# Optimization experiments

Measured on AMD Instinct MI355X. Metric: run time of the kernel, lower is better.

The kernel has to match this reference:

```python
import jax, jax.numpy as jnp
import numpy as np

N, F_IN, H, C, E = 100000, 512, 16, 40, 3200000
EPS = 1e-5


def setup_inputs() -> dict:
    key = jax.random.key(0)
    ks = jax.random.split(key, 8)
    x = jax.random.normal(ks[0], (N, F_IN), dtype=jnp.float32)
    edge_index = jax.random.randint(ks[1], (2, E), 0, N, dtype=jnp.int64)
    s1 = 1.0 / np.sqrt(F_IN)
    s2 = 1.0 / np.sqrt(H)
    W1 = jax.random.uniform(ks[2], (F_IN, H), jnp.float32, -s1, s1)
    b1 = jnp.zeros((H,), jnp.float32)
    W2 = jax.random.uniform(ks[3], (H, C), jnp.float32, -s2, s2)
    b2 = jnp.zeros((C,), jnp.float32)
    gamma = jnp.ones((H,), jnp.float32)
    beta = jnp.zeros((H,), jnp.float32)
    return {"x": x, "edge_index": edge_index, "W1": W1, "b1": b1,
            "W2": W2, "b2": b2, "gamma": gamma, "beta": beta}


def gcn_conv(x, edge_index, W, b):
    # PyG GCNConv: linear transform, add self-loops, symmetric normalization,
    # scatter-add aggregation at target nodes (edge_index[1]).
    xw = x @ W  # [N, out]
    loops = jnp.arange(N, dtype=edge_index.dtype)
    row = jnp.concatenate([edge_index[0], loops])  # sources
    col = jnp.concatenate([edge_index[1], loops])  # targets
    deg = jax.ops.segment_sum(jnp.ones_like(col, dtype=xw.dtype), col, num_segments=N)
    dis = jnp.where(deg > 0, jax.lax.rsqrt(deg), 0.0)
    norm = dis[row] * dis[col]  # [E+N]
    msgs = norm[:, None] * xw[row]
    out = jax.ops.segment_sum(msgs, col, num_segments=N)
    return out + b


def batch_norm(x, gamma, beta):
    mean = jnp.mean(x, axis=0)
    var = jnp.var(x, axis=0)
    return (x - mean) * jax.lax.rsqrt(var + EPS) * gamma + beta


def reference(x, edge_index, W1, b1, W2, b2, gamma, beta):
    h = jax.nn.relu(gcn_conv(x, edge_index, W1, b1))
    h = batch_norm(h, gamma, beta)
    # dropout omitted (deterministic reference / eval)
    h = gcn_conv(h, edge_index, W2, b2)
    return jax.nn.log_softmax(h, axis=1)
```

## Files before the change

### kernel.cpp

```cpp
#include <hip/hip_runtime.h>

#define NN 100000
#define FIN 512
#define HD 16
#define CD 40
#define NE 3200000
#define EPSV 1e-5f
#define NBUK 391
#define CAP 9216
#define CH 4096
#define NBLK_CNT ((NE + CH - 1) / CH)
#define NBLK_MM ((NN / 16 + 3) / 4)
#define NSTAT 256
#define SMEM_BYTES 37504

typedef __attribute__((ext_vector_type(8))) short short8;
typedef __attribute__((ext_vector_type(4))) float f32x4;

static __device__ __forceinline__ short f2bf(float f) {
  union { float f; unsigned u; } a; a.f = f;
  unsigned r = a.u + 0x7fffu + ((a.u >> 16) & 1u);
  return (short)(r >> 16);
}
static __device__ __forceinline__ float bf2f(unsigned short u) {
  union { unsigned u; float f; } a; a.u = (unsigned)u << 16; return a.f;
}
static __device__ __forceinline__ float2 bfp2f(unsigned p) {
  union { unsigned u; float f; } lo, hi;
  lo.u = p << 16;
  hi.u = p & 0xFFFF0000u;
  return make_float2(lo.f, hi.f);
}
static __device__ __forceinline__ void gload_lds(const float* g, float* l) {
  __builtin_amdgcn_global_load_lds(
      (const __attribute__((address_space(1))) void*)g,
      (__attribute__((address_space(3))) void*)l, 16, 0, 0);
}

__global__ void k_init(int* __restrict__ bkcur, int* __restrict__ gbase) {
  int i = threadIdx.x;
  if (i < NBUK) bkcur[i] = 0;
  if (i == 0) *gbase = 0;
}

__global__ void __launch_bounds__(256) k_fat(const int* __restrict__ ei,
                                             int* __restrict__ bkcur,
                                             unsigned* __restrict__ part,
                                             const float* __restrict__ x,
                                             const float* __restrict__ W1,
                                             float* __restrict__ xw) {
  __shared__ __align__(16) char smem_u[SMEM_BYTES];
  int t = threadIdx.x;
  if (blockIdx.x % 3 == 0) {
    unsigned* stg   = (unsigned*)smem_u;
    unsigned* spk   = stg + CH;
    int*      hist  = (int*)(spk + CH);
    int*      lbase = hist + NBUK;
    int*      gb    = lbase + NBUK + 1;
    int pb = blockIdx.x / 3;
    int e0 = pb * CH;
    int n = NE - e0; if (n > CH) n = CH;
    for (int i = t; i < NBUK; i += 256) hist[i] = 0;
    for (int i = t; i < n; i += 256) stg[i] = (unsigned)ei[NE + e0 + i];
    __syncthreads();
    for (int i = t; i < n; i += 256) atomicAdd(&hist[stg[i] >> 8], 1);
    __syncthreads();
    if (t < 64) {
      int c0 = t * 7;
      int loc[7]; int s = 0;
#pragma unroll
      for (int k = 0; k < 7; k++) {
        int idx = c0 + k;
        int v = (idx < NBUK) ? hist[idx] : 0;
        loc[k] = s; s += v;
      }
      int inc = s;
#pragma unroll
      for (int m = 1; m < 64; m <<= 1) {
        int u = __shfl_up(inc, m);
        if (t >= m) inc += u;
      }
      int base0 = inc - s;
#pragma unroll
      for (int k = 0; k < 7; k++) {
        int idx = c0 + k;
        if (idx < NBUK) lbase[idx] = base0 + loc[k];
      }
      if (t == 63) lbase[NBUK] = base0 + s;
    }
    __syncthreads();
    for (int i = t; i < NBUK; i += 256) {
      int c = hist[i];
      gb[i] = (c > 0) ? atomicAdd(&bkcur[i], c) : 0;
    }
    __syncthreads();
    for (int i = t; i < NBUK; i += 256) hist[i] = lbase[i];
    __syncthreads();
    for (int i = t; i < n; i += 256) {
      unsigned tg = stg[i];
      int b = tg >> 8;
      int pos = atomicAdd(&hist[b], 1);
      spk[pos] = (unsigned)ei[e0 + i] | ((tg & 255u) << 20);
    }
    __syncthreads();
    for (int b = t; b < NBUK; b += 256) {
      int s0 = lbase[b], s1 = lbase[b + 1];
      for (int j = s0; j < s1; j++) stg[j] = (unsigned)b;
    }
    __syncthreads();
    for (int i = t; i < n; i += 256) {
      int b = (int)stg[i];
      int slot = gb[b] + (i - lbase[b]);
      if (slot < CAP) part[(size_t)b * CAP + slot] = spk[i];
    }
  } else {
    int mb = blockIdx.x - blockIdx.x / 3 - 1;
    int wave = t >> 6;
    int lane = t & 63;
    int tile = mb * 4 + wave;
    int row0 = tile * 16;
    if (row0 >= NN) return;
    int lr = lane & 15;
    int kg = lane >> 4;
    float* xs = (float*)smem_u + wave * 2048;

    short8 bfrag[16];
#pragma unroll
    for (int s = 0; s < 16; s++) {
      int kbase = s * 32 + kg * 8;
      short8 bf;
#pragma unroll
      for (int i = 0; i < 8; i++) bf[i] = f2bf(W1[(kbase + i) * HD + lr]);
      bfrag[s] = bf;
    }

    const float* xbase = x + (size_t)row0 * FIN;
    int rr = lane >> 4;
    int pos = lane & 15;
#define STAGE(c)                                                         \
    {                                                                    \
      float* dst = xs + ((c) & 1) * 1024;                                \
      _Pragma("unroll")                                                  \
      for (int j = 0; j < 4; j++) {                                      \
        int row = j * 4 + rr;                                            \
        int u = (pos - row) & 15;                                        \
        gload_lds(xbase + (size_t)row * FIN + (c) * 64 + u * 4,          \
                  dst + j * 256);                                        \
      }                                                                  \
    }

    STAGE(0);
    STAGE(1);
    f32x4 acc = {0.f, 0.f, 0.f, 0.f};
#pragma unroll
    for (int c = 0; c < 8; c++) {
      if (c < 7) { asm volatile("s_waitcnt vmcnt(4)" ::: "memory"); }
      else       { asm volatile("s_waitcnt vmcnt(0)" ::: "memory"); }
      __builtin_amdgcn_sched_barrier(0);
      const float* bufp = xs + (c & 1) * 1024;
#pragma unroll
      for (int s2 = 0; s2 < 2; s2++) {
        int lu0 = s2 * 8 + 2 * kg;
        f32x4 u0 = *(const f32x4*)(bufp + lr * 64 + ((lu0 + lr) & 15) * 4);
        f32x4 u1 = *(const f32x4*)(bufp + lr * 64 + ((lu0 + 1 + lr) & 15) * 4);
        short8 af;
        af[0] = f2bf(u0.x); af[1] = f2bf(u0.y); af[2] = f2bf(u0.z); af[3] = f2bf(u0.w);
        af[4] = f2bf(u1.x); af[5] = f2bf(u1.y); af[6] = f2bf(u1.z); af[7] = f2bf(u1.w);
        acc = __builtin_amdgcn_mfma_f32_16x16x32_bf16(af, bfrag[c * 2 + s2], acc, 0, 0, 0);
      }
      __builtin_amdgcn_sched_barrier(0);
      if (c < 6) STAGE(c + 2);
    }
#undef STAGE
#pragma unroll
    for (int i = 0; i < 4; i++)
      xw[(size_t)(row0 + kg * 4 + i) * HD + lr] = acc[i];
  }
}

__global__ void __launch_bounds__(1024) k_bucket(const int* __restrict__ bkcur,
                                                 const unsigned* __restrict__ part,
                                                 const float* __restrict__ xw,
                                                 int* __restrict__ gbase,
                                                 int* __restrict__ off,
                                                 int* __restrict__ offe,
                                                 float* __restrict__ dis,
                                                 unsigned short* __restrict__ y1b,
                                                 int* __restrict__ srcs) {
  __shared__ unsigned ssrc[CAP];
  __shared__ int lh[256];
  __shared__ int lb[256];
  __shared__ int base_s;
  int b = blockIdx.x, t = threadIdx.x;
  int cnt = bkcur[b]; if (cnt > CAP) cnt = CAP;
  const unsigned* bp = part + (size_t)b * CAP;
  if (t < 256) lh[t] = 0;
  __syncthreads();
  for (int i = t; i < cnt; i += 1024) atomicAdd(&lh[(bp[i] >> 20) & 255], 1);
  __syncthreads();
  int h = 0;
  if (t < 256) { h = lh[t]; lb[t] = h; }
  __syncthreads();
  for (int d = 1; d < 256; d <<= 1) {
    int u = (t < 256 && t >= d) ? lb[t - d] : 0;
    __syncthreads();
    if (t < 256) lb[t] += u;
    __syncthreads();
  }
  if (t == 255) base_s = atomicAdd(gbase, lb[255]);
  __syncthreads();
  int base = base_s;
  if (t < 256) {
    int excl = lb[t] - h;
    int node = (b << 8) + t;
    if (node < NN) {
      off[node] = base + excl;
      offe[node] = base + excl + h;
      float d = rsqrtf((float)(1 + h));
      dis[node] = d;
      const f32x4* xp = (const f32x4*)(xw + (size_t)node * HD);
      f32x4 v0 = xp[0] * d, v1 = xp[1] * d, v2 = xp[2] * d, v3 = xp[3] * d;
      short8 r0, r1;
      r0[0] = f2bf(v0.x); r0[1] = f2bf(v0.y); r0[2] = f2bf(v0.z); r0[3] = f2bf(v0.w);
      r0[4] = f2bf(v1.x); r0[5] = f2bf(v1.y); r0[6] = f2bf(v1.z); r0[7] = f2bf(v1.w);
      r1[0] = f2bf(v2.x); r1[1] = f2bf(v2.y); r1[2] = f2bf(v2.z); r1[3] = f2bf(v2.w);
      r1[4] = f2bf(v3.x); r1[5] = f2bf(v3.y); r1[6] = f2bf(v3.z); r1[7] = f2bf(v3.w);
      short8* yp = (short8*)(y1b + (size_t)node * HD);
      yp[0] = r0; yp[1] = r1;
    }
    lh[t] = excl;
  }
  __syncthreads();
  for (int i = t; i < cnt; i += 1024) {
    unsigned p = bp[i];
    int pos = atomicAdd(&lh[(p >> 20) & 255], 1);
    ssrc[pos] = p & 0xFFFFFu;
  }
  __syncthreads();
  for (int i = t; i < cnt; i += 1024) srcs[base + i] = (int)ssrc[i];
}

__global__ void __launch_bounds__(256) k_g1(const int* __restrict__ off,
                                            const int* __restrict__ offe,
                                            const int* __restrict__ srcs,
                                            const float* __restrict__ dis,
                                            const unsigned short* __restrict__ y1b,
                                            const float* __restrict__ b1,
                                            float* __restrict__ h) {
  int node = (blockIdx.x * blockDim.x + threadIdx.x) >> 6;
  if (node >= NN) return;
  int lane = threadIdx.x & 63;
  int cp = lane & 7;
  int g = lane >> 3;
  int start = off[node], end = offe[node];
  const unsigned* y1u = (const unsigned*)y1b;
  float ax = 0.f, ay = 0.f;
  int i = start + g;
  for (; i + 24 < end; i += 32) {
    int r0 = srcs[i];
    int r1 = srcs[i + 8];
    int r2 = srcs[i + 16];
    int r3 = srcs[i + 24];
    float2 p0 = bfp2f(y1u[(size_t)r0 * 8 + cp]);
    float2 p1 = bfp2f(y1u[(size_t)r1 * 8 + cp]);
    float2 p2 = bfp2f(y1u[(size_t)r2 * 8 + cp]);
    float2 p3 = bfp2f(y1u[(size_t)r3 * 8 + cp]);
    ax += (p0.x + p1.x) + (p2.x + p3.x);
    ay += (p0.y + p1.y) + (p2.y + p3.y);
  }
  for (; i < end; i += 8) {
    float2 p = bfp2f(y1u[(size_t)srcs[i] * 8 + cp]);
    ax += p.x; ay += p.y;
  }
#pragma unroll
  for (int m = 8; m < 64; m <<= 1) {
    ax += __shfl_xor(ax, m);
    ay += __shfl_xor(ay, m);
  }
  if (g == 0) {
    float d = dis[node];
    float2 pn = bfp2f(y1u[(size_t)node * 8 + cp]);
    float vx = d * (pn.x + ax) + b1[2 * cp];
    float vy = d * (pn.y + ay) + b1[2 * cp + 1];
    float2* hp = (float2*)(h + (size_t)node * HD);
    hp[cp] = make_float2(fmaxf(vx, 0.f), fmaxf(vy, 0.f));
  }
}

__global__ void __launch_bounds__(256) k_stats(const float* __restrict__ h,
                                               float* __restrict__ partial) {
  __shared__ float wsum[4][32];
  int stride = gridDim.x * blockDim.x;
  int t0 = blockIdx.x * blockDim.x + threadIdx.x;
  f32x4 s = {0.f, 0.f, 0.f, 0.f}, s2 = {0.f, 0.f, 0.f, 0.f};
  for (int t = t0; t < NN * 4; t += stride) {
    f32x4 v = ((const f32x4*)h)[t];
    s += v; s2 += v * v;
  }
#pragma unroll
  for (int m = 4; m < 64; m <<= 1) {
    s.x += __shfl_xor(s.x, m);  s.y += __shfl_xor(s.y, m);
    s.z += __shfl_xor(s.z, m);  s.w += __shfl_xor(s.w, m);
    s2.x += __shfl_xor(s2.x, m); s2.y += __shfl_xor(s2.y, m);
    s2.z += __shfl_xor(s2.z, m); s2.w += __shfl_xor(s2.w, m);
  }
  int wave = threadIdx.x >> 6, lane = threadIdx.x & 63;
  if (lane < 4) {
    int cb = lane * 4;
    wsum[wave][cb + 0] = s.x;  wsum[wave][cb + 1] = s.y;
    wsum[wave][cb + 2] = s.z;  wsum[wave][cb + 3] = s.w;
    wsum[wave][16 + cb + 0] = s2.x; wsum[wave][16 + cb + 1] = s2.y;
    wsum[wave][16 + cb + 2] = s2.z; wsum[wave][16 + cb + 3] = s2.w;
  }
  __syncthreads();
  if (threadIdx.x < 32) {
    float a = ((wsum[0][threadIdx.x] + wsum[1][threadIdx.x]) +
               (wsum[2][threadIdx.x] + wsum[3][threadIdx.x]));
    partial[blockIdx.x * 32 + threadIdx.x] = a;
  }
}

__global__ void __launch_bounds__(256) k_y2(const float* __restrict__ h,
                                            const float* __restrict__ partial,
                                            const float* __restrict__ gamma,
                                            const float* __restrict__ beta,
                                            const float* __restrict__ dis,
                                            unsigned short* __restrict__ y2b) {
  __shared__ float raw[32];
  __shared__ float scs[16], shs[16];
  int j = threadIdx.x;
  if (j < 32) {
    float a = 0.f;
    for (int b = 0; b < NSTAT; b++) a += partial[b * 32 + j];
    raw[j] = a;
  }
  __syncthreads();
  if (j < 16) {
    float mean = raw[j] * (1.0f / NN);
    float var = raw[16 + j] * (1.0f / NN) - mean * mean;
    float inv = rsqrtf(var + EPSV);
    float sc = gamma[j] * inv;
    scs[j] = sc;
    shs[j] = beta[j] - mean * sc;
  }
  __syncthreads();
  int node = blockIdx.x * blockDim.x + j;
  if (node >= NN) return;
  float d = dis[node];
  const f32x4* hp = (const f32x4*)(h + (size_t)node * HD);
  const f32x4* scp = (const f32x4*)scs;
  const f32x4* shp = (const f32x4*)shs;
  f32x4 v0 = (hp[0] * scp[0] + shp[0]) * d;
  f32x4 v1 = (hp[1] * scp[1] + shp[1]) * d;
  f32x4 v2 = (hp[2] * scp[2] + shp[2]) * d;
  f32x4 v3 = (hp[3] * scp[3] + shp[3]) * d;
  short8 r0, r1;
  r0[0] = f2bf(v0.x); r0[1] = f2bf(v0.y); r0[2] = f2bf(v0.z); r0[3] = f2bf(v0.w);
  r0[4] = f2bf(v1.x); r0[5] = f2bf(v1.y); r0[6] = f2bf(v1.z); r0[7] = f2bf(v1.w);
  r1[0] = f2bf(v2.x); r1[1] = f2bf(v2.y); r1[2] = f2bf(v2.z); r1[3] = f2bf(v2.w);
  r1[4] = f2bf(v3.x); r1[5] = f2bf(v3.y); r1[6] = f2bf(v3.z); r1[7] = f2bf(v3.w);
  short8* yp = (short8*)(y2b + (size_t)node * HD);
  yp[0] = r0; yp[1] = r1;
}

__global__ void __launch_bounds__(256) k_g2(const int* __restrict__ off,
                                            const int* __restrict__ offe,
                                            const int* __restrict__ srcs,
                                            const float* __restrict__ dis,
                                            const unsigned short* __restrict__ y2b,
                                            const float* __restrict__ W2,
                                            const float* __restrict__ b2,
                                            float* __restrict__ out) {
  int node = (blockIdx.x * blockDim.x + threadIdx.x) >> 6;
  if (node >= NN) return;
  int lane = threadIdx.x & 63;
  int cp = lane & 7;
  int g = lane >> 3;
  int start = off[node], end = offe[node];
  const unsigned* y2u = (const unsigned*)y2b;
  float ax = 0.f, ay = 0.f;
  int i = start + g;
  for (; i + 24 < end; i += 32) {
    int r0 = srcs[i];
    int r1 = srcs[i + 8];
    int r2 = srcs[i + 16];
    int r3 = srcs[i + 24];
    float2 p0 = bfp2f(y2u[(size_t)r0 * 8 + cp]);
    float2 p1 = bfp2f(y2u[(size_t)r1 * 8 + cp]);
    float2 p2 = bfp2f(y2u[(size_t)r2 * 8 + cp]);
    float2 p3 = bfp2f(y2u[(size_t)r3 * 8 + cp]);
    ax += (p0.x + p1.x) + (p2.x + p3.x);
    ay += (p0.y + p1.y) + (p2.y + p3.y);
  }
  for (; i < end; i += 8) {
    float2 p = bfp2f(y2u[(size_t)srcs[i] * 8 + cp]);
    ax += p.x; ay += p.y;
  }
#pragma unroll
  for (int m = 8; m < 64; m <<= 1) {
    ax += __shfl_xor(ax, m);
    ay += __shfl_xor(ay, m);
  }
  float d = dis[node];
  float2 pn = bfp2f(y2u[(size_t)node * 8 + cp]);
  float rx = d * (pn.x + ax);
  float ry = d * (pn.y + ay);
  int cls = lane;
  float z = (cls < CD) ? b2[cls] : 0.f;
#pragma unroll
  for (int k = 0; k < 8; k++) {
    float rkx = __shfl(rx, k);
    float rky = __shfl(ry, k);
    if (cls < CD) {
      z += rkx * W2[(2 * k) * CD + cls];
      z += rky * W2[(2 * k + 1) * CD + cls];
    }
  }
  float zz = (cls < CD) ? z : -1e30f;
#pragma unroll
  for (int m = 1; m < 64; m <<= 1) zz = fmaxf(zz, __shfl_xor(zz, m));
  float e = (cls < CD) ? __expf(z - zz) : 0.f;
#pragma unroll
  for (int m = 1; m < 64; m <<= 1) e += __shfl_xor(e, m);
  float l = __logf(e) + zz;
  if (cls < CD) out[(size_t)node * CD + cls] = z - l;
}

extern "C" void kernel_launch(void* const* d_in, const int* in_sizes, int n_in,
                              void* d_out, int out_size, void* d_ws, size_t ws_size,
                              hipStream_t stream) {
  const float* x     = (const float*)d_in[0];
  const int*   ei    = (const int*)d_in[1];
  const float* W1    = (const float*)d_in[2];
  const float* b1    = (const float*)d_in[3];
  const float* W2    = (const float*)d_in[4];
  const float* b2    = (const float*)d_in[5];
  const float* gamma = (const float*)d_in[6];
  const float* beta  = (const float*)d_in[7];
  float* out = (float*)d_out;

  float* ws = (float*)d_ws;
  float*          dis     = ws;
  float*          partial = ws + NN;
  float*          xw      = partial + NSTAT * 32;
  unsigned short* y1b     = (unsigned short*)(xw + (size_t)NN * HD);
  float*          h       = (float*)(y1b + (size_t)NN * HD);
  unsigned short* y2b     = (unsigned short*)(h + (size_t)NN * HD);
  int*            off     = (int*)(y2b + (size_t)NN * HD);
  int*            offe    = off + NN;
  int*            srcs    = offe + NN;
  int*            bkcur   = srcs + NE;
  int*            gbase   = bkcur + NBUK;
  unsigned*       part    = (unsigned*)(gbase + 1);

  const int nblk_n   = (NN + 255) / 256;
  const int nblk_gw  = (NN * 64 + 255) / 256;
  const int nblk_fat = NBLK_CNT + NBLK_MM;

  k_init<<<1, 512, 0, stream>>>(bkcur, gbase);
  k_fat<<<nblk_fat, 256, 0, stream>>>(ei, bkcur, part, x, W1, xw);
  k_bucket<<<NBUK, 1024, 0, stream>>>(bkcur, part, xw, gbase, off, offe, dis, y1b, srcs);
  k_g1<<<nblk_gw, 256, 0, stream>>>(off, offe, srcs, dis, y1b, b1, h);
  k_stats<<<NSTAT, 256, 0, stream>>>(h, partial);
  k_y2<<<nblk_n, 256, 0, stream>>>(h, partial, gamma, beta, dis, y2b);
  k_g2<<<nblk_gw, 256, 0, stream>>>(off, offe, srcs, dis, y2b, W2, b2, out);
}
```

Measured before the change: 215.6 us.

## Shrink fused kernel shared memory: direct atomic scatter and smaller x staging chunks

The edge-partition blocks drop the local prefix-scan and staging pass. They now reserve global bucket offsets per block and scatter each edge directly using a shared atomic slot counter, so spk, lbase and gb are no longer needed. The matmul blocks stage 32-column chunks of x, down from 64, in a smaller double buffer and run 16 pipeline steps with a tighter vmcnt. Both changes cut shared memory per block roughly in half to allow more resident blocks. The cost is less locally coalesced global writes to part, since writes are no longer grouped by bucket, and shallower prefetch per stage.

```diff
diff --git a/kernel.cpp b/kernel.cpp
--- a/kernel.cpp
+++ b/kernel.cpp
@@ -12,7 +12,7 @@
 #define NBLK_CNT ((NE + CH - 1) / CH)
 #define NBLK_MM ((NN / 16 + 3) / 4)
 #define NSTAT 256
-#define SMEM_BYTES 37504
+#define SMEM_BYTES 17952
 
 typedef __attribute__((ext_vector_type(8))) short short8;
 typedef __attribute__((ext_vector_type(4))) float f32x4;
@@ -52,11 +52,8 @@
   __shared__ __align__(16) char smem_u[SMEM_BYTES];
   int t = threadIdx.x;
   if (blockIdx.x % 3 == 0) {
-    unsigned* stg   = (unsigned*)smem_u;
-    unsigned* spk   = stg + CH;
-    int*      hist  = (int*)(spk + CH);
-    int*      lbase = hist + NBUK;
-    int*      gb    = lbase + NBUK + 1;
+    unsigned* stg  = (unsigned*)smem_u;
+    int*      hist = (int*)(stg + CH);
     int pb = blockIdx.x / 3;
     int e0 = pb * CH;
     int n = NE - e0; if (n > CH) n = CH;
@@ -65,53 +62,17 @@
     __syncthreads();
     for (int i = t; i < n; i += 256) atomicAdd(&hist[stg[i] >> 8], 1);
     __syncthreads();
-    if (t < 64) {
-      int c0 = t * 7;
-      int loc[7]; int s = 0;
-#pragma unroll
-      for (int k = 0; k < 7; k++) {
-        int idx = c0 + k;
-        int v = (idx < NBUK) ? hist[idx] : 0;
-        loc[k] = s; s += v;
-      }
-      int inc = s;
-#pragma unroll
-      for (int m = 1; m < 64; m <<= 1) {
-        int u = __shfl_up(inc, m);
-        if (t >= m) inc += u;
-      }
-      int base0 = inc - s;
-#pragma unroll
-      for (int k = 0; k < 7; k++) {
-        int idx = c0 + k;
-        if (idx < NBUK) lbase[idx] = base0 + loc[k];
-      }
-      if (t == 63) lbase[NBUK] = base0 + s;
-    }
-    __syncthreads();
     for (int i = t; i < NBUK; i += 256) {
       int c = hist[i];
-      gb[i] = (c > 0) ? atomicAdd(&bkcur[i], c) : 0;
-    }
-    __syncthreads();
-    for (int i = t; i < NBUK; i += 256) hist[i] = lbase[i];
+      hist[i] = (c > 0) ? atomicAdd(&bkcur[i], c) : 0;
+    }
     __syncthreads();
     for (int i = t; i < n; i += 256) {
       unsigned tg = stg[i];
       int b = tg >> 8;
-      int pos = atomicAdd(&hist[b], 1);
-      spk[pos] = (unsigned)ei[e0 + i] | ((tg & 255u) << 20);
-    }
-    __syncthreads();
-    for (int b = t; b < NBUK; b += 256) {
-      int s0 = lbase[b], s1 = lbase[b + 1];
-      for (int j = s0; j < s1; j++) stg[j] = (unsigned)b;
-    }
-    __syncthreads();
-    for (int i = t; i < n; i += 256) {
-      int b = (int)stg[i];
-      int slot = gb[b] + (i - lbase[b]);
-      if (slot < CAP) part[(size_t)b * CAP + slot] = spk[i];
+      int slot = atomicAdd(&hist[b], 1);
+      if (slot < CAP)
+        part[(size_t)b * CAP + slot] = (unsigned)ei[e0 + i] | ((tg & 255u) << 20);
     }
   } else {
     int mb = blockIdx.x - blockIdx.x / 3 - 1;
@@ -122,7 +83,7 @@
     if (row0 >= NN) return;
     int lr = lane & 15;
     int kg = lane >> 4;
-    float* xs = (float*)smem_u + wave * 2048;
+    float* xs = (float*)smem_u + wave * 1024;
 
     short8 bfrag[16];
 #pragma unroll
@@ -135,16 +96,16 @@
     }
 
     const float* xbase = x + (size_t)row0 * FIN;
-    int rr = lane >> 4;
-    int pos = lane & 15;
+    int rr8 = lane >> 3;
+    int pos = lane & 7;
 #define STAGE(c)                                                         \
     {                                                                    \
-      float* dst = xs + ((c) & 1) * 1024;                                \
+      float* dst = xs + ((c) & 1) * 512;                                 \
       _Pragma("unroll")                                                  \
-      for (int j = 0; j < 4; j++) {                                      \
-        int row = j * 4 + rr;                                            \
-        int u = (pos - row) & 15;                                        \
-        gload_lds(xbase + (size_t)row * FIN + (c) * 64 + u * 4,          \
+      for (int j = 0; j < 2; j++) {                                      \
+        int row = j * 8 + rr8;                                           \
+        int u = (pos - row) & 7;                                         \
+        gload_lds(xbase + (size_t)row * FIN + (c) * 32 + u * 4,          \
                   dst + j * 256);                                        \
       }                                                                  \
     }
@@ -153,23 +114,19 @@
     STAGE(1);
     f32x4 acc = {0.f, 0.f, 0.f, 0.f};
 #pragma unroll
-    for (int c = 0; c < 8; c++) {
-      if (c < 7) { asm volatile("s_waitcnt vmcnt(4)" ::: "memory"); }
-      else       { asm volatile("s_waitcnt vmcnt(0)" ::: "memory"); }
+    for (int s = 0; s < 16; s++) {
+      if (s < 15) { asm volatile("s_waitcnt vmcnt(2)" ::: "memory"); }
+      else        { asm volatile("s_waitcnt vmcnt(0)" ::: "memory"); }
       __builtin_amdgcn_sched_barrier(0);
-      const float* bufp = xs + (c & 1) * 1024;
-#pragma unroll
-      for (int s2 = 0; s2 < 2; s2++) {
-        int lu0 = s2 * 8 + 2 * kg;
-        f32x4 u0 = *(const f32x4*)(bufp + lr * 64 + ((lu0 + lr) & 15) * 4);
-        f32x4 u1 = *(const f32x4*)(bufp + lr * 64 + ((lu0 + 1 + lr) & 15) * 4);
-        short8 af;
-        af[0] = f2bf(u0.x); af[1] = f2bf(u0.y); af[2] = f2bf(u0.z); af[3] = f2bf(u0.w);
-        af[4] = f2bf(u1.x); af[5] = f2bf(u1.y); af[6] = f2bf(u1.z); af[7] = f2bf(u1.w);
-        acc = __builtin_amdgcn_mfma_f32_16x16x32_bf16(af, bfrag[c * 2 + s2], acc, 0, 0, 0);
-      }
+      const float* bufp = xs + (s & 1) * 512;
+      f32x4 u0 = *(const f32x4*)(bufp + lr * 32 + ((2 * kg + lr) & 7) * 4);
+      f32x4 u1 = *(const f32x4*)(bufp + lr * 32 + ((2 * kg + 1 + lr) & 7) * 4);
+      short8 af;
+      af[0] = f2bf(u0.x); af[1] = f2bf(u0.y); af[2] = f2bf(u0.z); af[3] = f2bf(u0.w);
+      af[4] = f2bf(u1.x); af[5] = f2bf(u1.y); af[6] = f2bf(u1.z); af[7] = f2bf(u1.w);
+      acc = __builtin_amdgcn_mfma_f32_16x16x32_bf16(af, bfrag[s], acc, 0, 0, 0);
       __builtin_amdgcn_sched_barrier(0);
-      if (c < 6) STAGE(c + 2);
+      if (s < 14) STAGE(s + 2);
     }
 #undef STAGE
 #pragma unroll
```

Result: slower. 228.4 us (+5.9%).
